# Performance work log

Hardware: AMD Instinct MI355X
Metric: run time of the kernel (lower is better)

The kernel has to match this reference:

```python
import jax, jax.numpy as jnp
import numpy as np

B, S, D, H = 32, 512, 1024, 16
DK = D // H


def _xavier(key, shape):
    fan_in, fan_out = shape[1], shape[0]
    limit = float(np.sqrt(6.0 / (fan_in + fan_out)))
    return jax.random.uniform(key, shape, jnp.float32, -limit, limit)


def setup_inputs() -> dict:
    key = jax.random.key(0)
    ks = jax.random.split(key, 5)
    Q = jax.random.normal(ks[0], (B, S, D), jnp.float32)
    length = jax.random.randint(ks[1], (B,), 1, S + 1)  # valid key counts in [1, S]
    Wq = _xavier(ks[2], (D, D))
    Wk = _xavier(ks[3], (D, D))
    Wv = _xavier(ks[4], (D, D))
    bq = jnp.zeros((D,), jnp.float32)
    bk = jnp.zeros((D,), jnp.float32)
    bv = jnp.zeros((D,), jnp.float32)
    return {"Q": Q, "Wq": Wq, "bq": bq, "Wk": Wk, "bk": bk, "Wv": Wv, "bv": bv, "length": length}


def reference(Q, Wq, bq, Wk, bk, Wv, bv, length):
    b, s, d = Q.shape
    # QKV projections (self-attention: K = V = Q input)
    q = (Q @ Wq.T + bq).reshape(b, s, H, DK).transpose(0, 2, 1, 3)  # [B,H,S,DK]
    k = (Q @ Wk.T + bk).reshape(b, s, H, DK).transpose(0, 2, 1, 3)
    v = (Q @ Wv.T + bv).reshape(b, s, H, DK).transpose(0, 2, 1, 3)
    scores = jnp.einsum("bhqd,bhkd->bhqk", q, k) / jnp.sqrt(jnp.float32(DK))
    scores = jnp.exp(scores)  # NOTE: raw exp, no max-subtraction (faithful to source)
    # multiplicative post-exp key mask: key j valid iff j < length[b]
    mask = (jnp.arange(s)[None, :] < length[:, None]).astype(scores.dtype)  # [B,S]
    scores = scores * mask[:, None, None, :]
    attn = scores / (jnp.sum(scores, axis=-1, keepdims=True) + 1e-8)
    context = jnp.einsum("bhqk,bhkd->bhqd", attn, v)  # [B,H,S,DK]
    context = context.transpose(0, 2, 1, 3).reshape(b, s, H * DK)
    return context, attn
```

## Files before the change

kernel.cpp:

```cpp
#include <hip/hip_runtime.h>
#include <hip/hip_bf16.h>
#include <stdint.h>

#define NB 32
#define NS 512
#define ND 1024
#define NH 16
#define NDK 64

typedef unsigned short u16t;
typedef __bf16 bf16x8 __attribute__((ext_vector_type(8)));
typedef float f32x4 __attribute__((ext_vector_type(4)));
typedef u16t u16x8 __attribute__((ext_vector_type(8)));
typedef u16t u16x4 __attribute__((ext_vector_type(4)));

__device__ __forceinline__ u16t f2bf(float f) {
    uint32_t u = __float_as_uint(f);
    u += 0x7FFFu + ((u >> 16) & 1u);
    return (u16t)(u >> 16);
}

__device__ __forceinline__ void gload_lds16(const u16t* g, u16t* l) {
    __builtin_amdgcn_global_load_lds(
        (const __attribute__((address_space(1))) unsigned int*)g,
        (__attribute__((address_space(3))) unsigned int*)l, 16, 0, 0);
}

__global__ __launch_bounds__(256) void cast_kernel(
    const float4* __restrict__ Q, const float4* __restrict__ Wq,
    const float4* __restrict__ Wk, const float4* __restrict__ Wv,
    u16t* __restrict__ X, u16t* __restrict__ Wc)
{
    const int64_t NQ = 16777216 / 4;
    const int64_t NW = 1048576 / 4;
    const int64_t total = NQ + 3 * NW;
    for (int64_t i = (int64_t)blockIdx.x * 256 + threadIdx.x; i < total;
         i += (int64_t)gridDim.x * 256) {
        float4 v;
        u16t* dst;
        if (i < NQ) {
            v = Q[i];
            dst = X + i * 4;
        } else {
            int64_t j = i - NQ;
            int sel = (int)(j / NW);
            int64_t t = j % NW;
            v = (sel == 0 ? Wq : sel == 1 ? Wk : Wv)[t];
            dst = Wc + (sel * NW + t) * 4;
        }
        u16x4 o;
        o.x = f2bf(v.x); o.y = f2bf(v.y); o.z = f2bf(v.z); o.w = f2bf(v.w);
        *(u16x4*)dst = o;
    }
}

__global__ __launch_bounds__(256) void gemm_qkv(
    const u16t* __restrict__ X, const u16t* __restrict__ Wc,
    const float* __restrict__ bq, const float* __restrict__ bk,
    const float* __restrict__ bv,
    u16t* __restrict__ Qp, u16t* __restrict__ Kp, u16t* __restrict__ Vp)
{
    __shared__ __align__(16) u16t As[128 * 32];
    __shared__ __align__(16) u16t Bs[128 * 32];
    const int tid = threadIdx.x;
    const int lane = tid & 63, wave = tid >> 6;
    const int cl = lane & 15, g4 = lane >> 4;
    const int m0 = blockIdx.x * 128;
    const int n0 = blockIdx.y * 128;
    const int wm = (wave & 1) * 64, wn = (wave >> 1) * 64;

    f32x4 acc[4][4] = {};

    const int r0 = tid >> 2, sg0 = tid & 3;
    const int r1 = r0 + 64;
    const u16t* xrow0 = X  + (size_t)(m0 + r0) * 1024 + sg0 * 8;
    const u16t* xrow1 = X  + (size_t)(m0 + r1) * 1024 + sg0 * 8;
    const u16t* wrow0 = Wc + (size_t)(n0 + r0) * 1024 + sg0 * 8;
    const u16t* wrow1 = Wc + (size_t)(n0 + r1) * 1024 + sg0 * 8;
    u16t* asd0 = &As[r0 * 32 + sg0 * 8];
    u16t* asd1 = &As[r1 * 32 + sg0 * 8];
    u16t* bsd0 = &Bs[r0 * 32 + sg0 * 8];
    u16t* bsd1 = &Bs[r1 * 32 + sg0 * 8];

    for (int kt = 0; kt < 1024; kt += 32) {
        __syncthreads();
        gload_lds16(xrow0 + kt, asd0);
        gload_lds16(xrow1 + kt, asd1);
        gload_lds16(wrow0 + kt, bsd0);
        gload_lds16(wrow1 + kt, bsd1);
        __syncthreads();

        bf16x8 af[4], bf_[4];
#pragma unroll
        for (int t = 0; t < 4; ++t) {
            af[t]  = *(const bf16x8*)&As[(wm + t * 16 + cl) * 32 + g4 * 8];
            bf_[t] = *(const bf16x8*)&Bs[(wn + t * 16 + cl) * 32 + g4 * 8];
        }
#pragma unroll
        for (int mt = 0; mt < 4; ++mt)
#pragma unroll
            for (int nt = 0; nt < 4; ++nt)
                acc[mt][nt] = __builtin_amdgcn_mfma_f32_16x16x32_bf16(
                    af[mt], bf_[nt], acc[mt][nt], 0, 0, 0);
    }

    const int w = n0 >> 10;
    const float* bias = (w == 0) ? bq : (w == 1) ? bk : bv;
    u16t* outp = (w == 0) ? Qp : (w == 1) ? Kp : Vp;
    const float scale = (w == 0) ? 0.125f : 1.0f;
    const int nfbase = (n0 & 1023) + wn;
#pragma unroll
    for (int nt = 0; nt < 4; ++nt) {
        const int nf = nfbase + nt * 16 + cl;
        const int h = nf >> 6, dk = nf & 63;
        const float bval = bias[nf];
#pragma unroll
        for (int mt = 0; mt < 4; ++mt) {
#pragma unroll
            for (int r = 0; r < 4; ++r) {
                const int m = m0 + wm + mt * 16 + g4 * 4 + r;
                const int b = m >> 9, s = m & 511;
                float val = (acc[mt][nt][r] + bval) * scale;
                outp[((size_t)(b * NH + h) * NS + s) * NDK + dk] = f2bf(val);
            }
        }
    }
}

__global__ __launch_bounds__(256) void transpose_v(
    const u16t* __restrict__ Vp, u16t* __restrict__ Vt)
{
    __shared__ __align__(16) u16t T[64 * 72];
    const int bh = blockIdx.x;
    const int sc = blockIdx.y;
    const u16t* src = Vp + (size_t)bh * NS * NDK + (size_t)sc * 64 * NDK;
    u16t* dst = Vt + (size_t)bh * NDK * NS + sc * 64;

#pragma unroll
    for (int i = 0; i < 2; ++i) {
        int c = threadIdx.x + i * 256;
        int row = c >> 3, sg = c & 7;
        *(u16x8*)&T[row * 72 + sg * 8] = *(const u16x8*)&src[row * 64 + sg * 8];
    }
    __syncthreads();
#pragma unroll
    for (int i = 0; i < 2; ++i) {
        int c = threadIdx.x + i * 256;
        int dk = c >> 3, sg = c & 7;
        u16x8 v;
#pragma unroll
        for (int j = 0; j < 8; ++j) v[j] = T[(sg * 8 + j) * 72 + dk];
        *(u16x8*)&dst[(size_t)dk * NS + sg * 8] = v;
    }
}

__global__ __launch_bounds__(256) void attn_kernel(
    const u16t* __restrict__ Qp, const u16t* __restrict__ Kp,
    const u16t* __restrict__ Vt, const int* __restrict__ length,
    float* __restrict__ ctx, float* __restrict__ attn)
{
    __shared__ __align__(16) u16t Pst[4][16 * 40];
    const int tid = threadIdx.x, lane = tid & 63, wave = tid >> 6;
    const int cl = lane & 15, g4 = lane >> 4;
    const int raw = blockIdx.x;
    const int bh = ((raw >> 6) << 3) | (raw & 7);
    const int qt = (raw >> 3) & 7;
    const int b = bh >> 4;
    const int len = length[b];
    const int nkt = (len + 15) >> 4;
    const int ng  = (len + 31) >> 5;
    const int qbase = qt * 64 + wave * 16;

    const u16t* qptr = Qp + (size_t)bh * NS * NDK + (size_t)qbase * NDK;
    const u16t* kptr = Kp + (size_t)bh * NS * NDK;
    const u16t* vtptr = Vt + (size_t)bh * NDK * NS;

    const bf16x8 aq0 = *(const bf16x8*)&qptr[cl * 64 + g4 * 8];
    const bf16x8 aq1 = *(const bf16x8*)&qptr[cl * 64 + 32 + g4 * 8];

    f32x4 E[32];
    float rs[4] = {0.f, 0.f, 0.f, 0.f};
#pragma unroll
    for (int kt = 0; kt < 32; ++kt) {
        if (kt < nkt) {
            const bf16x8 bk0 = *(const bf16x8*)&kptr[(kt * 16 + cl) * 64 + g4 * 8];
            const bf16x8 bk1 = *(const bf16x8*)&kptr[(kt * 16 + cl) * 64 + 32 + g4 * 8];
            f32x4 sc = {0.f, 0.f, 0.f, 0.f};
            sc = __builtin_amdgcn_mfma_f32_16x16x32_bf16(aq0, bk0, sc, 0, 0, 0);
            sc = __builtin_amdgcn_mfma_f32_16x16x32_bf16(aq1, bk1, sc, 0, 0, 0);
            const bool valid = (kt * 16 + cl) < len;
            f32x4 e;
#pragma unroll
            for (int r = 0; r < 4; ++r) {
                float ev = valid ? __expf(sc[r]) : 0.0f;
                e[r] = ev;
                rs[r] += ev;
            }
            E[kt] = e;
        } else {
            E[kt] = (f32x4){0.f, 0.f, 0.f, 0.f};
        }
    }

#pragma unroll
    for (int r = 0; r < 4; ++r) {
        float v = rs[r];
        v += __shfl_xor(v, 1);
        v += __shfl_xor(v, 2);
        v += __shfl_xor(v, 4);
        v += __shfl_xor(v, 8);
        rs[r] = 1.0f / (v + 1e-8f);
    }

    f32x4 cacc[4] = {};
    float* attnw = attn + ((size_t)bh * NS + qbase) * NS;
#pragma unroll
    for (int g = 0; g < 16; ++g) {
        if (g < ng) {
#pragma unroll
            for (int t = 0; t < 2; ++t) {
                const int kt = g * 2 + t;
#pragma unroll
                for (int r = 0; r < 4; ++r) {
                    const float a = E[kt][r] * rs[r];
                    attnw[(size_t)(g4 * 4 + r) * NS + kt * 16 + cl] = a;
                    Pst[wave][(g4 * 4 + r) * 40 + t * 16 + cl] = f2bf(a);
                }
            }
            const bf16x8 ap = *(const bf16x8*)&Pst[wave][cl * 40 + g4 * 8];
#pragma unroll
            for (int nt = 0; nt < 4; ++nt) {
                const bf16x8 bv = *(const bf16x8*)
                    &vtptr[(size_t)(nt * 16 + cl) * NS + g * 32 + g4 * 8];
                cacc[nt] = __builtin_amdgcn_mfma_f32_16x16x32_bf16(
                    ap, bv, cacc[nt], 0, 0, 0);
            }
        }
    }

    {
        const int zr = lane >> 2;
        const int zc = (lane & 3) * 4;
        const float4 z = {0.f, 0.f, 0.f, 0.f};
        for (int c = ng * 32; c < NS; c += 16)
            *(float4*)&attnw[(size_t)zr * NS + c + zc] = z;
    }

    float* cw = ctx + ((size_t)b * NS + qbase) * ND + (bh & 15) * NDK;
#pragma unroll
    for (int nt = 0; nt < 4; ++nt)
#pragma unroll
        for (int r = 0; r < 4; ++r)
            cw[(size_t)(g4 * 4 + r) * ND + nt * 16 + cl] = cacc[nt][r];
}

extern "C" void kernel_launch(void* const* d_in, const int* in_sizes, int n_in,
                              void* d_out, int out_size, void* d_ws, size_t ws_size,
                              hipStream_t stream)
{
    const float* Q   = (const float*)d_in[0];
    const float* Wq  = (const float*)d_in[1];
    const float* bq  = (const float*)d_in[2];
    const float* Wk  = (const float*)d_in[3];
    const float* bk  = (const float*)d_in[4];
    const float* Wv  = (const float*)d_in[5];
    const float* bv  = (const float*)d_in[6];
    const int* length = (const int*)d_in[7];

    float* ctx  = (float*)d_out;
    float* attn = (float*)d_out + 16777216;

    char* ws = (char*)d_ws;
    const size_t szX  = 33554432;
    const size_t szW  = 6291456;
    const size_t szP  = 33554432;

    u16t *X, *Wc, *Qp, *Kp, *Vp, *Vt;
    const size_t needA = szX + szW + 4 * szP;
    if (ws_size >= needA) {
        X  = (u16t*)(ws);
        Wc = (u16t*)(ws + szX);
        Qp = (u16t*)(ws + szX + szW);
        Kp = (u16t*)(ws + szX + szW + szP);
        Vp = (u16t*)(ws + szX + szW + 2 * szP);
        Vt = (u16t*)(ws + szX + szW + 3 * szP);
    } else {
        X  = (u16t*)(attn);
        Wc = (u16t*)((char*)attn + szX);
        Qp = (u16t*)(ws);
        Kp = (u16t*)(ws + szP);
        Vp = (u16t*)(ws + 2 * szP);
        Vt = (u16t*)(ws + 3 * szP);
    }

    cast_kernel<<<dim3(2048), dim3(256), 0, stream>>>(
        (const float4*)Q, (const float4*)Wq, (const float4*)Wk,
        (const float4*)Wv, X, Wc);

    gemm_qkv<<<dim3(128, 24), dim3(256), 0, stream>>>(
        X, Wc, bq, bk, bv, Qp, Kp, Vp);

    transpose_v<<<dim3(512, 8), dim3(256), 0, stream>>>(Vp, Vt);

    attn_kernel<<<dim3(4096), dim3(256), 0, stream>>>(
        Qp, Kp, Vt, length, ctx, attn);
}
```

Measured before the change: 953.9 us.

## Rewrite QKV GEMM with 256x256 tiles, 4-stage LDS pipeline and swizzles

```diff
diff --git a/kernel.cpp b/kernel.cpp
--- a/kernel.cpp
+++ b/kernel.cpp
@@ -54,71 +54,114 @@
     }
 }
 
-__global__ __launch_bounds__(256) void gemm_qkv(
+#define MF(m_, a_, n_, b_) \
+    acc[m_][n_] = __builtin_amdgcn_mfma_f32_16x16x32_bf16(a_, b_, acc[m_][n_], 0, 0, 0)
+
+__global__ __launch_bounds__(512, 2) void gemm_qkv(
     const u16t* __restrict__ X, const u16t* __restrict__ Wc,
     const float* __restrict__ bq, const float* __restrict__ bk,
     const float* __restrict__ bv,
     u16t* __restrict__ Qp, u16t* __restrict__ Kp, u16t* __restrict__ Vp)
 {
-    __shared__ __align__(16) u16t As[128 * 32];
-    __shared__ __align__(16) u16t Bs[128 * 32];
+    __shared__ __align__(16) u16t sm[65536];
     const int tid = threadIdx.x;
     const int lane = tid & 63, wave = tid >> 6;
     const int cl = lane & 15, g4 = lane >> 4;
-    const int m0 = blockIdx.x * 128;
-    const int n0 = blockIdx.y * 128;
-    const int wm = (wave & 1) * 64, wn = (wave >> 1) * 64;
-
-    f32x4 acc[4][4] = {};
-
-    const int r0 = tid >> 2, sg0 = tid & 3;
-    const int r1 = r0 + 64;
-    const u16t* xrow0 = X  + (size_t)(m0 + r0) * 1024 + sg0 * 8;
-    const u16t* xrow1 = X  + (size_t)(m0 + r1) * 1024 + sg0 * 8;
-    const u16t* wrow0 = Wc + (size_t)(n0 + r0) * 1024 + sg0 * 8;
-    const u16t* wrow1 = Wc + (size_t)(n0 + r1) * 1024 + sg0 * 8;
-    u16t* asd0 = &As[r0 * 32 + sg0 * 8];
-    u16t* asd1 = &As[r1 * 32 + sg0 * 8];
-    u16t* bsd0 = &Bs[r0 * 32 + sg0 * 8];
-    u16t* bsd1 = &Bs[r1 * 32 + sg0 * 8];
-
-    for (int kt = 0; kt < 1024; kt += 32) {
-        __syncthreads();
-        gload_lds16(xrow0 + kt, asd0);
-        gload_lds16(xrow1 + kt, asd1);
-        gload_lds16(wrow0 + kt, bsd0);
-        gload_lds16(wrow1 + kt, bsd1);
-        __syncthreads();
-
-        bf16x8 af[4], bf_[4];
-#pragma unroll
-        for (int t = 0; t < 4; ++t) {
-            af[t]  = *(const bf16x8*)&As[(wm + t * 16 + cl) * 32 + g4 * 8];
-            bf_[t] = *(const bf16x8*)&Bs[(wn + t * 16 + cl) * 32 + g4 * 8];
-        }
-#pragma unroll
-        for (int mt = 0; mt < 4; ++mt)
-#pragma unroll
-            for (int nt = 0; nt < 4; ++nt)
-                acc[mt][nt] = __builtin_amdgcn_mfma_f32_16x16x32_bf16(
-                    af[mt], bf_[nt], acc[mt][nt], 0, 0, 0);
+    const int wmRow = (wave >> 2) * 128;
+    const int wnCol = (wave & 3) * 64;
+
+    const int bid = blockIdx.x;
+    const int swz = (bid & 7) * 96 + (bid >> 3);
+    const int bx = swz / 12, by = swz % 12;
+    const int m0 = bx * 256, n0 = by * 256;
+
+    f32x4 acc[8][4] = {};
+
+    const int row0 = tid >> 2;
+    const int csw  = (tid & 3) ^ ((tid >> 3) & 3);
+    const u16t* pA0 = X  + (size_t)(m0 + row0) * 1024 + csw * 8;
+    const u16t* pA1 = pA0 + 128 * 1024;
+    const u16t* pB0 = Wc + (size_t)(n0 + row0) * 1024 + csw * 8;
+    const u16t* pB1 = pB0 + 128 * 1024;
+    const u16t* Xd  = X + tid * 8;
+
+    const int axor = (g4 ^ ((cl >> 1) & 3)) * 8;
+    const int aoff = (wmRow + cl) * 32 + axor;
+    const int boff = 32768 + (wnCol + cl) * 32 + axor;
+
+#pragma unroll
+    for (int p = 0; p < 3; ++p) {
+        gload_lds16(pA0 + p * 32, &sm[p * 8192 + tid * 8]);
+        gload_lds16(pA1 + p * 32, &sm[p * 8192 + 4096 + tid * 8]);
+        gload_lds16(pB0 + p * 32, &sm[32768 + p * 8192 + tid * 8]);
+        gload_lds16(pB1 + p * 32, &sm[32768 + p * 8192 + 4096 + tid * 8]);
+    }
+    asm volatile("s_waitcnt vmcnt(8)\n\ts_barrier" ::: "memory");
+
+    for (int t = 0; t < 32; ++t) {
+        const int base = (t & 3) * 8192;
+        const int tau = t + 3;
+        const bool real = tau < 32;
+        const int tb = (tau & 3) * 8192;
+
+        const bf16x8 a0 = *(const bf16x8*)&sm[base + aoff];
+        const bf16x8 a1 = *(const bf16x8*)&sm[base + aoff + 512];
+        const bf16x8 a2 = *(const bf16x8*)&sm[base + aoff + 1024];
+        const bf16x8 a3 = *(const bf16x8*)&sm[base + aoff + 1536];
+        const bf16x8 b0 = *(const bf16x8*)&sm[base + boff];
+        const bf16x8 b1 = *(const bf16x8*)&sm[base + boff + 512];
+        const bf16x8 b2 = *(const bf16x8*)&sm[base + boff + 1024];
+        const bf16x8 b3 = *(const bf16x8*)&sm[base + boff + 1536];
+        {
+            const u16t* s0 = real ? pA0 + tau * 32 : Xd;
+            const u16t* s1 = real ? pA1 + tau * 32 : Xd;
+            gload_lds16(s0, &sm[tb + tid * 8]);
+            gload_lds16(s1, &sm[tb + 4096 + tid * 8]);
+        }
+        asm volatile("s_barrier" ::: "memory");
+        __builtin_amdgcn_s_setprio(1);
+        MF(0, a0, 0, b0); MF(0, a0, 1, b1); MF(0, a0, 2, b2); MF(0, a0, 3, b3);
+        MF(1, a1, 0, b0); MF(1, a1, 1, b1); MF(1, a1, 2, b2); MF(1, a1, 3, b3);
+        MF(2, a2, 0, b0); MF(2, a2, 1, b1); MF(2, a2, 2, b2); MF(2, a2, 3, b3);
+        MF(3, a3, 0, b0); MF(3, a3, 1, b1); MF(3, a3, 2, b2); MF(3, a3, 3, b3);
+        __builtin_amdgcn_s_setprio(0);
+        asm volatile("s_barrier" ::: "memory");
+
+        const bf16x8 a4 = *(const bf16x8*)&sm[base + aoff + 2048];
+        const bf16x8 a5 = *(const bf16x8*)&sm[base + aoff + 2560];
+        const bf16x8 a6 = *(const bf16x8*)&sm[base + aoff + 3072];
+        const bf16x8 a7 = *(const bf16x8*)&sm[base + aoff + 3584];
+        {
+            const u16t* s0 = real ? pB0 + tau * 32 : Xd;
+            const u16t* s1 = real ? pB1 + tau * 32 : Xd;
+            gload_lds16(s0, &sm[32768 + tb + tid * 8]);
+            gload_lds16(s1, &sm[32768 + tb + 4096 + tid * 8]);
+        }
+        asm volatile("s_barrier" ::: "memory");
+        __builtin_amdgcn_s_setprio(1);
+        MF(4, a4, 0, b0); MF(4, a4, 1, b1); MF(4, a4, 2, b2); MF(4, a4, 3, b3);
+        MF(5, a5, 0, b0); MF(5, a5, 1, b1); MF(5, a5, 2, b2); MF(5, a5, 3, b3);
+        MF(6, a6, 0, b0); MF(6, a6, 1, b1); MF(6, a6, 2, b2); MF(6, a6, 3, b3);
+        MF(7, a7, 0, b0); MF(7, a7, 1, b1); MF(7, a7, 2, b2); MF(7, a7, 3, b3);
+        __builtin_amdgcn_s_setprio(0);
+        asm volatile("s_waitcnt vmcnt(8)\n\ts_barrier" ::: "memory");
     }
 
     const int w = n0 >> 10;
     const float* bias = (w == 0) ? bq : (w == 1) ? bk : bv;
     u16t* outp = (w == 0) ? Qp : (w == 1) ? Kp : Vp;
     const float scale = (w == 0) ? 0.125f : 1.0f;
-    const int nfbase = (n0 & 1023) + wn;
+    const int nfbase = (n0 & 1023) + wnCol;
 #pragma unroll
     for (int nt = 0; nt < 4; ++nt) {
         const int nf = nfbase + nt * 16 + cl;
         const int h = nf >> 6, dk = nf & 63;
         const float bval = bias[nf];
 #pragma unroll
-        for (int mt = 0; mt < 4; ++mt) {
+        for (int mt = 0; mt < 8; ++mt) {
 #pragma unroll
             for (int r = 0; r < 4; ++r) {
-                const int m = m0 + wm + mt * 16 + g4 * 4 + r;
+                const int m = m0 + wmRow + mt * 16 + g4 * 4 + r;
                 const int b = m >> 9, s = m & 511;
                 float val = (acc[mt][nt][r] + bval) * scale;
                 outp[((size_t)(b * NH + h) * NS + s) * NDK + dk] = f2bf(val);
@@ -297,7 +340,7 @@
         (const float4*)Q, (const float4*)Wq, (const float4*)Wk,
         (const float4*)Wv, X, Wc);
 
-    gemm_qkv<<<dim3(128, 24), dim3(256), 0, stream>>>(
+    gemm_qkv<<<dim3(768), dim3(512), 0, stream>>>(
         X, Wc, bq, bk, bv, Qp, Kp, Vp);
 
     transpose_v<<<dim3(512, 8), dim3(256), 0, stream>>>(Vp, Vt);
```

Measured after the change: 965.9 us. No clear change (+1.2%).
